# Performance work log

Measured on AMD Instinct MI355X. Metric: run time of the kernel, lower is better.

The kernel has to match this reference:

```python
import jax, jax.numpy as jnp
import numpy as np

D_MODEL = 1024
N_HEADS = 16
D_K = D_MODEL // N_HEADS


def setup_inputs() -> dict:
    key = jax.random.key(0)
    ks = jax.random.split(key, 12)
    B, S = 4, 2048
    sc = 1.0 / np.sqrt(D_MODEL)
    inp = {
        "query": jax.random.normal(ks[0], (B, S, D_MODEL), jnp.float32),
        "key": jax.random.normal(ks[1], (B, S, D_MODEL), jnp.float32),
        "value": jax.random.normal(ks[2], (B, S, D_MODEL), jnp.float32),
        "Wq": jax.random.normal(ks[3], (D_MODEL, D_MODEL), jnp.float32) * sc,
        "bq": jnp.zeros((D_MODEL,), jnp.float32),
        "Wk": jax.random.normal(ks[4], (D_MODEL, D_MODEL), jnp.float32) * sc,
        "bk": jnp.zeros((D_MODEL,), jnp.float32),
        "Wv": jax.random.normal(ks[5], (D_MODEL, D_MODEL), jnp.float32) * sc,
        "bv": jnp.zeros((D_MODEL,), jnp.float32),
        "Wo": jax.random.normal(ks[6], (D_MODEL, D_MODEL), jnp.float32) * sc,
        "bo": jnp.zeros((D_MODEL,), jnp.float32),
    }
    return inp


def _split_heads(x):
    B, S, _ = x.shape
    return x.reshape(B, S, N_HEADS, D_K).transpose(0, 2, 1, 3)  # [B,H,S,Dk]


def reference(query, key, value, Wq, bq, Wk, bk, Wv, bv, Wo, bo):
    q = _split_heads(query @ Wq.T + bq)
    k = _split_heads(key @ Wk.T + bk)
    v = _split_heads(value @ Wv.T + bv)
    scores = jnp.einsum("bhqd,bhkd->bhqk", q, k) / jnp.sqrt(jnp.float32(D_K))
    # Faithful to source: softmax over dim=1 (the HEAD axis), a quirk of the original.
    probs = jax.nn.softmax(scores, axis=1)
    attn = jnp.einsum("bhqk,bhkd->bhqd", probs, v)
    B, H, S, Dk = attn.shape
    combined = attn.transpose(0, 2, 1, 3).reshape(B, S, H * Dk)
    return combined @ Wo.T + bo
```

## Files before the change

kernel.cpp:

```cpp
#include <hip/hip_runtime.h>
#include <stdint.h>

typedef __attribute__((ext_vector_type(8))) short bf16x8;
typedef __attribute__((ext_vector_type(4))) float f32x4;
typedef __attribute__((ext_vector_type(4))) float fl4;
typedef __attribute__((ext_vector_type(4))) unsigned short u16x4;
typedef __attribute__((ext_vector_type(8))) unsigned short u16x8;

constexpr int SEQ = 2048;
constexpr int DMODEL = 1024;
constexpr int NH = 16;
constexpr int DKH = 64;
constexpr float SEXP = 0.18033688f;

__device__ __forceinline__ unsigned short f2bf(float x) {
  union { float f; uint32_t u; } c;
  c.f = x;
  uint32_t u = c.u;
  u += 0x7FFFu + ((u >> 16) & 1u);
  return (unsigned short)(u >> 16);
}

__device__ __forceinline__ float bf2f(unsigned short u) {
  union { uint32_t u; float f; } c;
  c.u = ((uint32_t)u) << 16;
  return c.f;
}

__device__ __forceinline__ uint32_t cvtpk(float lo, float hi) {
  uint32_t r;
  asm("v_cvt_pk_bf16_f32 %0, %1, %2" : "=v"(r) : "v"(lo), "v"(hi));
  return r;
}

#if __has_builtin(__builtin_amdgcn_exp2f)
__device__ __forceinline__ float fexp2(float x) { return __builtin_amdgcn_exp2f(x); }
#else
__device__ __forceinline__ float fexp2(float x) { return exp2f(x); }
#endif

__device__ __forceinline__ int swz(int row) { return (row & 3) ^ ((row >> 2) & 3); }

__device__ __forceinline__ void gload16(const unsigned short* g, unsigned short* l) {
  __builtin_amdgcn_global_load_lds((const __attribute__((address_space(1))) void*)g,
                                   (__attribute__((address_space(3))) void*)l, 16, 0, 0);
}

__global__ __launch_bounds__(256) void cvtk(
    const float* __restrict__ s0, const float* __restrict__ s1, const float* __restrict__ s2,
    unsigned short* __restrict__ d0, unsigned short* __restrict__ d1, unsigned short* __restrict__ d2) {
  const float* s = blockIdx.y == 0 ? s0 : blockIdx.y == 1 ? s1 : s2;
  unsigned short* d = blockIdx.y == 0 ? d0 : blockIdx.y == 1 ? d1 : d2;
  const size_t i = ((size_t)blockIdx.x * 256 + threadIdx.x) * 8;
  fl4 a = *(const fl4*)(s + i);
  fl4 c = *(const fl4*)(s + i + 4);
  u16x8 r;
#pragma unroll
  for (int j = 0; j < 4; ++j) { r[j] = f2bf(a[j]); r[4 + j] = f2bf(c[j]); }
  *(u16x8*)(d + i) = r;
}

__global__ __launch_bounds__(256) void cvt1(
    const float* __restrict__ s, unsigned short* __restrict__ d) {
  const size_t i = ((size_t)blockIdx.x * 256 + threadIdx.x) * 8;
  fl4 a = *(const fl4*)(s + i);
  fl4 c = *(const fl4*)(s + i + 4);
  u16x8 r;
#pragma unroll
  for (int j = 0; j < 4; ++j) { r[j] = f2bf(a[j]); r[4 + j] = f2bf(c[j]); }
  *(u16x8*)(d + i) = r;
}

template <int EPI>
__global__ __launch_bounds__(256, 2) void gemm3(
    const unsigned short* __restrict__ A, const unsigned short* __restrict__ Bb,
    const float* __restrict__ bias, void* __restrict__ Cp, float ascale) {
  constexpr int K = DMODEL;
  constexpr int N = DMODEL;
  __shared__ unsigned short As[2][128 * 32];
  __shared__ unsigned short Bs[2][128 * 32];
  const int tid = threadIdx.x;
  const int wave = tid >> 6, lane = tid & 63;
  const int g = lane >> 4, ln = lane & 15;
  const int o = blockIdx.x;
  const int x = o & 7, idx = o >> 3;
  const int r0 = (x * 8 + (idx & 7)) * 128;
  const int c0 = (idx >> 3) * 128;
  const int wr = (wave >> 1) * 64, wc = (wave & 1) * 64;

  f32x4 acc[4][4] = {};

  auto STAGE = [&](int buf, int kt) {
#pragma unroll
    for (int i = 0; i < 2; ++i) {
      const int row = i * 64 + (tid >> 2);
      const int cs = ((tid & 3) ^ swz(row)) * 8;
      gload16(A + (size_t)(r0 + row) * K + kt + cs, As[buf] + (i * 256 + wave * 64) * 8);
      gload16(Bb + (size_t)(c0 + row) * K + kt + cs, Bs[buf] + (i * 256 + wave * 64) * 8);
    }
  };

  STAGE(0, 0);
  __syncthreads();

  for (int t = 0; t < K / 32; ++t) {
    const int buf = t & 1;
    if (t + 1 < K / 32) STAGE(buf ^ 1, (t + 1) * 32);
    bf16x8 af[4], bfr[4];
#pragma unroll
    for (int m = 0; m < 4; ++m) {
      const int row = wr + m * 16 + ln;
      af[m] = *(const bf16x8*)(As[buf] + row * 32 + ((g ^ swz(row)) * 8));
    }
#pragma unroll
    for (int n = 0; n < 4; ++n) {
      const int row = wc + n * 16 + ln;
      bfr[n] = *(const bf16x8*)(Bs[buf] + row * 32 + ((g ^ swz(row)) * 8));
    }
#pragma unroll
    for (int m = 0; m < 4; ++m)
#pragma unroll
      for (int n = 0; n < 4; ++n)
        acc[m][n] = __builtin_amdgcn_mfma_f32_16x16x32_bf16(af[m], bfr[n], acc[m][n], 0, 0, 0);
    __syncthreads();
  }

#pragma unroll
  for (int m = 0; m < 4; ++m) {
    const int row = r0 + wr + m * 16 + g * 4;
#pragma unroll
    for (int n = 0; n < 4; ++n) {
      const int col = c0 + wc + n * 16 + ln;
      const float bv = bias[col];
      f32x4 v = acc[m][n];
      if (EPI == 2) {
        float* C = (float*)Cp;
#pragma unroll
        for (int r = 0; r < 4; ++r) C[(size_t)(row + r) * N + col] = (v[r] + bv) * ascale;
      } else if (EPI == 0) {
        unsigned short* C = (unsigned short*)Cp;
#pragma unroll
        for (int r = 0; r < 4; ++r) C[(size_t)(row + r) * N + col] = f2bf((v[r] + bv) * ascale);
      } else {
        unsigned short* Vt = (unsigned short*)Cp;
        const int bb = row >> 11, sl = row & 2047;
        const int h = col >> 6, d = col & 63;
        const int sp = (sl & ~31) | (((sl >> 2) & 3) << 3) | (((sl >> 4) & 1) << 2);
        u16x4 pk;
#pragma unroll
        for (int r = 0; r < 4; ++r) pk[r] = f2bf((v[r] + bv) * ascale);
        *(u16x4*)(Vt + ((size_t)((bb * NH + h) * DKH + d)) * SEQ + sp) = pk;
      }
    }
  }
}

__global__ __launch_bounds__(256, 3) void denomk(
    const unsigned short* __restrict__ Qp, const unsigned short* __restrict__ Kp,
    unsigned short* __restrict__ rDb) {
  __shared__ unsigned short Ks[2][128 * 64];
  const int tid = threadIdx.x, wave = tid >> 6, lane = tid & 63;
  const int g = lane >> 4, ln = lane & 15;
  const int o = blockIdx.x;
  const int l = (o & 7) * 256 + (o >> 3);
  const int b = l >> 9;
  const int qg = (l >> 4) & 31;
  const int kvg = l & 15;
  const int q0 = qg * 64, kvb = kvg * 128;
  const int kw = wave * 32;

  auto STAGE = [&](int buf, int h) {
#pragma unroll
    for (int i = 0; i < 4; ++i) {
      const int s = i * 256 + tid;
      const int row = s >> 3, c = s & 7;
      gload16(Kp + (size_t)(b * SEQ + kvb + row) * DMODEL + h * DKH + ((c ^ (row & 7)) * 8),
              Ks[buf] + (i * 256 + wave * 64) * 8);
    }
  };

  f32x4 psum[2][4] = {};

  STAGE(0, 0);
  __syncthreads();

  for (int h = 0; h < NH; ++h) {
    const int buf = h & 1;
    if (h + 1 < NH) STAGE(buf ^ 1, h + 1);
    bf16x8 qf[2][4];
#pragma unroll
    for (int ks = 0; ks < 2; ++ks)
#pragma unroll
      for (int n = 0; n < 4; ++n)
        qf[ks][n] = *(const bf16x8*)(Qp + (size_t)(b * SEQ + q0 + n * 16 + ln) * DMODEL + h * DKH + ks * 32 + g * 8);
    bf16x8 kf[2][2];
#pragma unroll
    for (int m = 0; m < 2; ++m)
#pragma unroll
      for (int ks = 0; ks < 2; ++ks) {
        const int r = kw + m * 16 + ln;
        const int cc = ks * 4 + g;
        kf[m][ks] = *(const bf16x8*)(Ks[buf] + r * 64 + ((cc ^ (r & 7)) * 8));
      }
    f32x4 s[2][4] = {};
#pragma unroll
    for (int m = 0; m < 2; ++m)
#pragma unroll
      for (int n = 0; n < 4; ++n) {
        s[m][n] = __builtin_amdgcn_mfma_f32_16x16x32_bf16(kf[m][0], qf[0][n], s[m][n], 0, 0, 0);
        s[m][n] = __builtin_amdgcn_mfma_f32_16x16x32_bf16(kf[m][1], qf[1][n], s[m][n], 0, 0, 0);
      }
#pragma unroll
    for (int m = 0; m < 2; ++m)
#pragma unroll
      for (int n = 0; n < 4; ++n)
#pragma unroll
        for (int r = 0; r < 4; ++r) psum[m][n][r] += fexp2(s[m][n][r]);
    __syncthreads();
  }

#pragma unroll
  for (int m = 0; m < 2; ++m)
#pragma unroll
    for (int n = 0; n < 4; ++n) {
      u16x4 st;
#pragma unroll
      for (int r = 0; r < 4; ++r) st[r] = f2bf(1.0f / psum[m][n][r]);
      *(u16x4*)(rDb + (size_t)(b * SEQ + q0 + n * 16 + ln) * SEQ + kvb + kw + m * 16 + g * 4) = st;
    }
}

__global__ __launch_bounds__(256, 4) void flashk(
    const unsigned short* __restrict__ Qp, const unsigned short* __restrict__ Kp,
    const unsigned short* __restrict__ Vt, const unsigned short* __restrict__ rDb,
    unsigned short* __restrict__ Ab) {
  __shared__ unsigned short Ks[2][32 * 128];
  __shared__ unsigned short Vs[2][128 * 32];
  const int tid = threadIdx.x, wave = tid >> 6, lane = tid & 63;
  const int g = lane >> 4, ln = lane & 15;
  const int o = blockIdx.x;
  const int l = (o & 7) * 128 + (o >> 3);
  const int b = l >> 8;
  const int hp = (l >> 5) & 7;
  const int qg0 = (l & 31) * 64;
  const int hl = wave >> 1, h = hp * 2 + hl;
  const int qg = qg0 + (wave & 1) * 32;

  bf16x8 qf[2][2];
#pragma unroll
  for (int ks = 0; ks < 2; ++ks)
#pragma unroll
    for (int n = 0; n < 2; ++n)
      qf[ks][n] = *(const bf16x8*)(Qp + (size_t)(b * SEQ + qg + n * 16 + ln) * DMODEL + h * DKH + ks * 32 + g * 8);

  f32x4 ao[4][2] = {};
  const size_t rbase0 = (size_t)(b * SEQ + qg + ln) * SEQ;

  auto STAGE = [&](int buf, int kv0) {
#pragma unroll
    for (int i = 0; i < 2; ++i) {
      const int s = i * 256 + tid;
      {
        const int row = s >> 4, c = s & 15;
        gload16(Kp + (size_t)(b * SEQ + kv0 + row) * DMODEL + hp * 128 + ((c ^ (row & 7)) * 8),
                Ks[buf] + (i * 256 + wave * 64) * 8);
      }
      {
        const int row = s >> 2, c = s & 3;
        gload16(Vt + ((size_t)((b * NH + hp * 2 + (row >> 6)) * DKH + (row & 63))) * SEQ + kv0 + ((c ^ (row & 3)) * 8),
                Vs[buf] + (i * 256 + wave * 64) * 8);
      }
    }
  };

  STAGE(0, 0);
  __syncthreads();

  for (int t = 0; t < SEQ / 32; ++t) {
    const int kv0 = t * 32, buf = t & 1;
    u16x4 rdq[2][2];
#pragma unroll
    for (int n = 0; n < 2; ++n)
#pragma unroll
      for (int m = 0; m < 2; ++m)
        rdq[n][m] = *(const u16x4*)(rDb + rbase0 + (size_t)(n * 16) * SEQ + kv0 + m * 16 + g * 4);
    if (t + 1 < SEQ / 32) STAGE(buf ^ 1, kv0 + 32);

    f32x4 s2[2][2] = {};
    __builtin_amdgcn_s_setprio(1);
#pragma unroll
    for (int m = 0; m < 2; ++m) {
      const int row = m * 16 + ln;
#pragma unroll
      for (int ks = 0; ks < 2; ++ks) {
        const int c = hl * 8 + ks * 4 + g;
        bf16x8 kf = *(const bf16x8*)(Ks[buf] + row * 128 + ((c ^ (row & 7)) * 8));
#pragma unroll
        for (int n = 0; n < 2; ++n)
          s2[m][n] = __builtin_amdgcn_mfma_f32_16x16x32_bf16(kf, qf[ks][n], s2[m][n], 0, 0, 0);
      }
    }
    __builtin_amdgcn_s_setprio(0);

    bf16x8 pfr[2];
#pragma unroll
    for (int n = 0; n < 2; ++n) {
      uint32_t dw[4];
#pragma unroll
      for (int m = 0; m < 2; ++m) {
        float p0 = fexp2(s2[m][n][0]) * bf2f(rdq[n][m][0]);
        float p1 = fexp2(s2[m][n][1]) * bf2f(rdq[n][m][1]);
        float p2 = fexp2(s2[m][n][2]) * bf2f(rdq[n][m][2]);
        float p3 = fexp2(s2[m][n][3]) * bf2f(rdq[n][m][3]);
        dw[m * 2 + 0] = cvtpk(p0, p1);
        dw[m * 2 + 1] = cvtpk(p2, p3);
      }
      union { uint32_t u[4]; bf16x8 v; } cv;
      cv.u[0] = dw[0]; cv.u[1] = dw[1]; cv.u[2] = dw[2]; cv.u[3] = dw[3];
      pfr[n] = cv.v;
    }

    __builtin_amdgcn_s_setprio(1);
#pragma unroll
    for (int dt = 0; dt < 4; ++dt) {
      const int vrow = hl * 64 + dt * 16 + ln;
      bf16x8 vf = *(const bf16x8*)(Vs[buf] + vrow * 32 + ((g ^ (vrow & 3)) * 8));
#pragma unroll
      for (int n = 0; n < 2; ++n)
        ao[dt][n] = __builtin_amdgcn_mfma_f32_16x16x32_bf16(vf, pfr[n], ao[dt][n], 0, 0, 0);
    }
    __builtin_amdgcn_s_setprio(0);
    __syncthreads();
  }

#pragma unroll
  for (int dt = 0; dt < 4; ++dt)
#pragma unroll
    for (int n = 0; n < 2; ++n) {
      u16x4 st;
#pragma unroll
      for (int r = 0; r < 4; ++r) st[r] = f2bf(ao[dt][n][r]);
      *(u16x4*)(Ab + (size_t)(b * SEQ + qg + n * 16 + ln) * DMODEL + h * DKH + dt * 16 + g * 4) = st;
    }
}

extern "C" void kernel_launch(void* const* d_in, const int* in_sizes, int n_in,
                              void* d_out, int out_size, void* d_ws, size_t ws_size,
                              hipStream_t stream) {
  (void)in_sizes; (void)n_in; (void)out_size; (void)ws_size;
  const float* query = (const float*)d_in[0];
  const float* key   = (const float*)d_in[1];
  const float* value = (const float*)d_in[2];
  const float* Wq = (const float*)d_in[3];
  const float* bq = (const float*)d_in[4];
  const float* Wk = (const float*)d_in[5];
  const float* bk = (const float*)d_in[6];
  const float* Wv = (const float*)d_in[7];
  const float* bv = (const float*)d_in[8];
  const float* Wo = (const float*)d_in[9];
  const float* bo = (const float*)d_in[10];

  uint8_t* ws = (uint8_t*)d_ws;
  const size_t SZ = (size_t)4 * SEQ * DMODEL * 2;
  const size_t WSZ = (size_t)DMODEL * DMODEL;
  unsigned short* Xv = (unsigned short*)(ws);
  unsigned short* Qp = (unsigned short*)(ws);
  unsigned short* Wob = (unsigned short*)(ws);
  unsigned short* Kp = (unsigned short*)(ws + SZ);
  unsigned short* Vt = (unsigned short*)(ws + 2 * SZ);
  unsigned short* Ab = (unsigned short*)(ws + 3 * SZ);
  unsigned short* Wqb = Ab;
  unsigned short* Wkb = Ab + WSZ;
  unsigned short* Wvb = Ab + 2 * WSZ;
  unsigned short* Xq = (unsigned short*)d_out;
  unsigned short* Xk = (unsigned short*)d_out + (size_t)4 * SEQ * DMODEL;
  unsigned short* rDb = (unsigned short*)d_out;

  cvtk<<<dim3(4096, 3), 256, 0, stream>>>(query, key, value, Xq, Xk, Xv);
  cvtk<<<dim3(512, 3), 256, 0, stream>>>(Wq, Wk, Wv, Wqb, Wkb, Wvb);
  gemm3<1><<<512, 256, 0, stream>>>(Xv, Wvb, bv, Vt, 1.0f);
  gemm3<0><<<512, 256, 0, stream>>>(Xq, Wqb, bq, Qp, SEXP);
  gemm3<0><<<512, 256, 0, stream>>>(Xk, Wkb, bk, Kp, 1.0f);
  denomk<<<2048, 256, 0, stream>>>(Qp, Kp, rDb);
  flashk<<<1024, 256, 0, stream>>>(Qp, Kp, Vt, rDb, Ab);
  cvt1<<<512, 256, 0, stream>>>(Wo, Wob);
  gemm3<2><<<512, 256, 0, stream>>>(Ab, Wob, bo, (float*)d_out, 1.0f);
}
```

Measured before the change: 433.9 us.

## Remap flash kernel blocks to one head with four query subtiles

New measurement: 747.8 us. +72.3%, slower.

```diff
diff --git a/kernel.cpp b/kernel.cpp
--- a/kernel.cpp
+++ b/kernel.cpp
@@ -230,46 +230,42 @@
     }
 }
 
-__global__ __launch_bounds__(256, 4) void flashk(
+__global__ __launch_bounds__(256, 8) void flashk(
     const unsigned short* __restrict__ Qp, const unsigned short* __restrict__ Kp,
     const unsigned short* __restrict__ Vt, const unsigned short* __restrict__ rDb,
     unsigned short* __restrict__ Ab) {
-  __shared__ unsigned short Ks[2][32 * 128];
-  __shared__ unsigned short Vs[2][128 * 32];
+  __shared__ unsigned short Ks[2][32 * 64];
+  __shared__ unsigned short Vs[2][64 * 32];
   const int tid = threadIdx.x, wave = tid >> 6, lane = tid & 63;
   const int g = lane >> 4, ln = lane & 15;
   const int o = blockIdx.x;
   const int l = (o & 7) * 128 + (o >> 3);
   const int b = l >> 8;
-  const int hp = (l >> 5) & 7;
-  const int qg0 = (l & 31) * 64;
-  const int hl = wave >> 1, h = hp * 2 + hl;
-  const int qg = qg0 + (wave & 1) * 32;
+  const int h = (l >> 4) & 15;
+  const int q0 = (l & 15) * 128 + wave * 32;
 
   bf16x8 qf[2][2];
 #pragma unroll
   for (int ks = 0; ks < 2; ++ks)
 #pragma unroll
     for (int n = 0; n < 2; ++n)
-      qf[ks][n] = *(const bf16x8*)(Qp + (size_t)(b * SEQ + qg + n * 16 + ln) * DMODEL + h * DKH + ks * 32 + g * 8);
+      qf[ks][n] = *(const bf16x8*)(Qp + (size_t)(b * SEQ + q0 + n * 16 + ln) * DMODEL + h * DKH + ks * 32 + g * 8);
 
   f32x4 ao[4][2] = {};
-  const size_t rbase0 = (size_t)(b * SEQ + qg + ln) * SEQ;
+  const size_t rbase0 = (size_t)(b * SEQ + q0 + ln) * SEQ;
+  const size_t kbase = (size_t)(b * SEQ) * DMODEL + h * DKH;
+  const size_t vbase = (size_t)((b * NH + h) * DKH) * SEQ;
 
   auto STAGE = [&](int buf, int kv0) {
-#pragma unroll
-    for (int i = 0; i < 2; ++i) {
-      const int s = i * 256 + tid;
-      {
-        const int row = s >> 4, c = s & 15;
-        gload16(Kp + (size_t)(b * SEQ + kv0 + row) * DMODEL + hp * 128 + ((c ^ (row & 7)) * 8),
-                Ks[buf] + (i * 256 + wave * 64) * 8);
-      }
-      {
-        const int row = s >> 2, c = s & 3;
-        gload16(Vt + ((size_t)((b * NH + hp * 2 + (row >> 6)) * DKH + (row & 63))) * SEQ + kv0 + ((c ^ (row & 3)) * 8),
-                Vs[buf] + (i * 256 + wave * 64) * 8);
-      }
+    {
+      const int row = tid >> 3, c = tid & 7;
+      gload16(Kp + kbase + (size_t)(kv0 + row) * DMODEL + ((c ^ (row & 7)) * 8),
+              Ks[buf] + (wave * 64) * 8);
+    }
+    {
+      const int row = tid >> 2, c = tid & 3;
+      gload16(Vt + vbase + (size_t)row * SEQ + kv0 + ((c ^ (row & 3)) * 8),
+              Vs[buf] + (wave * 64) * 8);
     }
   };
 
@@ -293,8 +289,8 @@
       const int row = m * 16 + ln;
 #pragma unroll
       for (int ks = 0; ks < 2; ++ks) {
-        const int c = hl * 8 + ks * 4 + g;
-        bf16x8 kf = *(const bf16x8*)(Ks[buf] + row * 128 + ((c ^ (row & 7)) * 8));
+        const int cc = ks * 4 + g;
+        bf16x8 kf = *(const bf16x8*)(Ks[buf] + row * 64 + ((cc ^ (row & 7)) * 8));
 #pragma unroll
         for (int n = 0; n < 2; ++n)
           s2[m][n] = __builtin_amdgcn_mfma_f32_16x16x32_bf16(kf, qf[ks][n], s2[m][n], 0, 0, 0);
@@ -323,7 +319,7 @@
     __builtin_amdgcn_s_setprio(1);
 #pragma unroll
     for (int dt = 0; dt < 4; ++dt) {
-      const int vrow = hl * 64 + dt * 16 + ln;
+      const int vrow = dt * 16 + ln;
       bf16x8 vf = *(const bf16x8*)(Vs[buf] + vrow * 32 + ((g ^ (vrow & 3)) * 8));
 #pragma unroll
       for (int n = 0; n < 2; ++n)
@@ -340,7 +336,7 @@
       u16x4 st;
 #pragma unroll
       for (int r = 0; r < 4; ++r) st[r] = f2bf(ao[dt][n][r]);
-      *(u16x4*)(Ab + (size_t)(b * SEQ + qg + n * 16 + ln) * DMODEL + h * DKH + dt * 16 + g * 4) = st;
+      *(u16x4*)(Ab + (size_t)(b * SEQ + q0 + n * 16 + ln) * DMODEL + h * DKH + dt * 16 + g * 4) = st;
     }
 }
 
```
